# Optimization experiments

Hardware: AMD Instinct MI355X
Metric: run time of the kernel (lower is better)

Reference implementation:

```python
import jax, jax.numpy as jnp
import numpy as np

B, C, H = 4, 64, 48
HEADS, BSWIN = 2, 4
BIG = [3, 6, 12, 24]      # big window edge per scale (cubic)
SMALL = [1, 2, 4, 8]      # small (pool) window edge per scale
NH = 3                    # small windows per big window per dim (= big/small)
L = NH ** 3               # tokens per big window after pooling
CPH = C // (HEADS * BSWIN)  # channels per head per scale = 8


def _rel_pos_index():
    coords = np.stack(np.meshgrid(*([np.arange(NH)] * 3), indexing='ij')).reshape(3, -1)
    rel = coords[:, :, None] - coords[:, None, :] + (NH - 1)
    span = 2 * NH - 1
    return jnp.asarray(rel[0] * span * span + rel[1] * span + rel[2])  # (L, L) int

REL_IDX = _rel_pos_index()


def _interp_matrix(n_in, n_out):
    # 1D linear interpolation matrix, align_corners=True (matches F.interpolate)
    if n_out == n_in:
        return jnp.eye(n_in, dtype=jnp.float32)
    pos = jnp.arange(n_out, dtype=jnp.float32) * (n_in - 1) / (n_out - 1)
    i0 = jnp.clip(jnp.floor(pos).astype(jnp.int32), 0, n_in - 2)
    w = pos - i0.astype(jnp.float32)
    r = jnp.arange(n_out)
    m = jnp.zeros((n_out, n_in), jnp.float32)
    return m.at[r, i0].add(1.0 - w).at[r, i0 + 1].add(w)


def _gather(x):
    # x: (B, C, H, H, H) -> (B, HEADS, sum_N, L, CPH)
    b = x.shape[0]
    x = x.reshape(b, BSWIN, HEADS, CPH, H, H, H)
    parts, Ns = [], []
    for i in range(BSWIN):
        bw, sw = BIG[i], SMALL[i]
        N1 = H // bw
        xi = x[:, i].reshape(b, HEADS, CPH, N1, NH, sw, N1, NH, sw, N1, NH, sw)
        xi = xi.max(axis=(5, 8, 11))  # max-pool each small window
        # (b, head, c, Nh, nh, Nw, nw, Nd, nd) -> b head (Nh Nw Nd) (nh nw nd) c
        xi = xi.transpose(0, 1, 3, 5, 7, 4, 6, 8, 2)
        parts.append(xi.reshape(b, HEADS, N1 ** 3, L, CPH))
        Ns.append(N1)
    return jnp.concatenate(parts, axis=2), Ns


def _scatter(attn, Ns):
    # attn: (B, HEADS, sum_N, L, CPH) -> (B, C, H, H, H)
    b = attn.shape[0]
    outs, idx = [], 0
    for i in range(BSWIN):
        bw, sw = BIG[i], SMALL[i]
        N1 = Ns[i]
        N = N1 ** 3
        o = attn[:, :, idx:idx + N].reshape(b, HEADS, N, NH, NH, NH, CPH)
        M = _interp_matrix(NH, bw)  # trilinear upsample by small window size
        o = jnp.einsum('bhnijkc,pi,qj,rk->bhnpqrc', o, M, M, M)
        o = o.reshape(b, HEADS, N1, N1, N1, bw, bw, bw, CPH)
        # b head Nh Nw Nd wh ww wd c -> b head c (Nh wh) (Nw ww) (Nd wd)
        o = o.transpose(0, 1, 8, 2, 5, 3, 6, 4, 7).reshape(b, HEADS, CPH, H, H, H)
        outs.append(o)
        idx += N
    out = jnp.stack(outs, axis=1)  # b bswin head c h w d
    return out.reshape(b, C, H, H, H)


def _attention(q, k, v, rpb_table):
    c = q.shape[-1]
    scores = jnp.einsum('bhNmc,bhNnc->bhNmn', q, k) / jnp.sqrt(jnp.asarray(c, q.dtype))
    w = jax.nn.softmax(scores, axis=-1)
    bias = rpb_table[REL_IDX].transpose(2, 0, 1)  # (head, L, L), added POST-softmax
    w = w + bias[None, :, None]
    return jnp.einsum('bhNmn,bhNnc->bhNmc', w, v)


def setup_inputs() -> dict:
    key = jax.random.key(0)
    kq, kk, kv, kp = jax.random.split(key, 4)
    shp = (B, C, H, H, H)
    return {
        'query': jax.random.normal(kq, shp, jnp.float32),
        'key': jax.random.normal(kk, shp, jnp.float32),
        'value': jax.random.normal(kv, shp, jnp.float32),
        'rpb_table': jax.random.normal(kp, ((2 * NH - 1) ** 3, HEADS), jnp.float32) * 0.02,
    }


def reference(query, key, value, rpb_table):
    q, Ns = _gather(query)
    k, _ = _gather(key)
    v, _ = _gather(value)
    attn = _attention(q, k, v, rpb_table)
    return _scatter(attn, Ns)
```

## Files before the change

kernel.cpp:

```cpp
#include <hip/hip_runtime.h>


static constexpr long S1 = 4L * 48 * 24 * 24 * 24;
static constexpr long S2 = 4L * 32 * 12 * 12 * 12;
static constexpr long S3 = 4L * 16 * 6 * 6 * 6;

template <int OUTW>
__global__ void pool_kernel(const float* __restrict__ in0,
                            const float* __restrict__ in1,
                            const float* __restrict__ in2,
                            float* __restrict__ out, long outStride,
                            int Cin, int chOff, int Cout, int Din, int n)
{
    const float* in = blockIdx.y == 0 ? in0 : (blockIdx.y == 1 ? in1 : in2);
    float* o = out + (long)blockIdx.y * outStride;
    const int Dout = Din >> 1;
    const int QX = Dout / OUTW;
    int idx = blockIdx.x * blockDim.x + threadIdx.x;
    if (idx >= n) return;
    int qx = idx % QX;
    int t = idx / QX;
    int y = t % Dout; t /= Dout;
    int z = t % Dout; t /= Dout;
    int c = t % Cout;
    int b = t / Cout;
    const float* p = in + ((((long)b * Cin + c + chOff) * Din + 2 * z) * Din + 2 * y) * Din
                        + qx * (2 * OUTW);
    const float* rows[4] = { p, p + Din, p + (long)Din * Din, p + (long)Din * Din + Din };

    float v[4][2 * OUTW];
#pragma unroll
    for (int r = 0; r < 4; r++) {
#pragma unroll
        for (int j = 0; j < OUTW / 2; j++) {
            float4 f = *(const float4*)(rows[r] + 4 * j);
            v[r][4 * j + 0] = f.x; v[r][4 * j + 1] = f.y;
            v[r][4 * j + 2] = f.z; v[r][4 * j + 3] = f.w;
        }
    }
    float res[OUTW];
#pragma unroll
    for (int i = 0; i < OUTW; i++) {
        float m0 = fmaxf(v[0][2 * i], v[0][2 * i + 1]);
        float m1 = fmaxf(v[1][2 * i], v[1][2 * i + 1]);
        float m2 = fmaxf(v[2][2 * i], v[2][2 * i + 1]);
        float m3 = fmaxf(v[3][2 * i], v[3][2 * i + 1]);
        res[i] = fmaxf(fmaxf(m0, m1), fmaxf(m2, m3));
    }
    long oaddr = ((((long)b * Cout + c) * Dout + z) * Dout + y) * Dout + qx * OUTW;
    if (OUTW == 4) {
        *(float4*)(o + oaddr) = make_float4(res[0], res[1], res[2], res[3 % OUTW]);
    } else {
        *(float2*)(o + oaddr) = make_float2(res[0], res[1]);
    }
}

template <int S>
__global__ void attn_kernel(const float* __restrict__ qsrc,
                            const float* __restrict__ ksrc,
                            const float* __restrict__ vsrc,
                            const float* __restrict__ rpb,
                            float* __restrict__ attnOut)
{
    constexpr int N1 = (S == 0 ? 16 : S == 1 ? 8 : S == 2 ? 4 : 2);
    constexpr int D  = 3 * N1;
    constexpr int Cs = (S == 0 ? 64 : S == 1 ? 48 : S == 2 ? 32 : 16);
    constexpr int scaleOff = (S == 0 ? 0 : S == 1 ? 4096 : S == 2 ? 4608 : 4672);
    constexpr int VEC = (S == 3 ? 2 : 4);
    constexpr int SEG = 3 * D;
    constexpr int NSEG = 72;
    constexpr int TOTV = NSEG * SEG / VEC;

    __shared__ float tile[N1][3][27][8];
    __shared__ float bias_lds[2][27][27];

    const int b = blockIdx.z;
    const int head = blockIdx.y;
    const int Wz = blockIdx.x / N1;
    const int Wy = blockIdx.x % N1;

    for (int i = threadIdx.x; i < 2 * 729; i += blockDim.x) {
        int h = i / 729;
        int mn = i % 729;
        int m = mn / 27, n = mn % 27;
        int mi = m / 9, mj = (m / 3) % 3, mk = m % 3;
        int ni = n / 9, nj = (n / 3) % 3, nk = n % 3;
        int ridx = (mi - ni + 2) * 25 + (mj - nj + 2) * 5 + (mk - nk + 2);
        bias_lds[h][m][n] = rpb[ridx * 2 + h];
    }

    for (int i = threadIdx.x; i < TOTV; i += blockDim.x) {
        int seg = i / (SEG / VEC);
        int off = (i % (SEG / VEC)) * VEC;
        int tz = seg / 24;
        int rem = seg % 24;
        int cph = rem / 3;
        int zt = rem % 3;
        const float* src = tz == 0 ? qsrc : (tz == 1 ? ksrc : vsrc);
        long base = ((((long)b * Cs + head * 8 + cph) * D + (3 * Wz + zt)) * D + 3 * Wy) * (long)D;
        const float* sp = src + base + off;
        float vals[VEC];
        if (VEC == 4) {
            float4 f = *(const float4*)sp;
            vals[0] = f.x; vals[1] = f.y; vals[2] = f.z; vals[3 % VEC] = f.w;
        } else {
            float2 f = *(const float2*)sp;
            vals[0] = f.x; vals[1] = f.y;
        }
#pragma unroll
        for (int j = 0; j < VEC; j++) {
            int f = off + j;
            int r = f / D;
            int x = f % D;
            tile[x / 3][tz][zt * 9 + r * 3 + (x % 3)][cph] = vals[j];
        }
    }
    __syncthreads();

    const int wx = threadIdx.x >> 5;
    const int lane = threadIdx.x & 31;
    if (lane >= 27) return;
    const int m = lane;

    float qr[8];
#pragma unroll
    for (int c = 0; c < 8; c++) qr[c] = tile[wx][0][m][c];

    float s[27];
    float mx = -1e30f;
#pragma unroll
    for (int n = 0; n < 27; n++) {
        float acc = 0.f;
#pragma unroll
        for (int c = 0; c < 8; c++) acc += qr[c] * tile[wx][1][n][c];
        acc *= 0.35355339059327373f;
        s[n] = acc;
        mx = fmaxf(mx, acc);
    }
    float sum = 0.f;
#pragma unroll
    for (int n = 0; n < 27; n++) {
        s[n] = __expf(s[n] - mx);
        sum += s[n];
    }
    float rs = 1.0f / sum;

    float o[8] = {0, 0, 0, 0, 0, 0, 0, 0};
#pragma unroll
    for (int n = 0; n < 27; n++) {
        float wgt = s[n] * rs + bias_lds[head][m][n];
#pragma unroll
        for (int c = 0; c < 8; c++) o[c] += wgt * tile[wx][2][n][c];
    }

    const int win = (Wz * N1 + Wy) * N1 + wx;
    float* dst = attnOut + (((long)(b * 2 + head) * 4680 + scaleOff + win) * 27 + m) * 8;
    *(float4*)(dst) = make_float4(o[0], o[1], o[2], o[3]);
    *(float4*)(dst + 4) = make_float4(o[4], o[5], o[6], o[7]);
}

template <int S>
__global__ void scatter_s(const float* __restrict__ attn, float* __restrict__ out)
{
    constexpr int bw = (S == 0 ? 3 : S == 1 ? 6 : S == 2 ? 12 : 24);
    constexpr int N1 = 48 / bw;
    constexpr int scaleOff = (S == 0 ? 0 : S == 1 ? 4096 : S == 2 ? 4608 : 4672);
    constexpr int CZ = (S == 0 ? 3 : S == 1 ? 3 : 1);
    constexpr int NZC = bw / CZ;
    constexpr int LDSF = N1 * 216;
    constexpr int NF4 = CZ * bw * 8 * 12;

    __shared__ float lds[LDSF];

    const int b = blockIdx.z;
    const int head = blockIdx.y;
    int t = blockIdx.x;
    const int zc = t % NZC; t /= NZC;
    const int Wy = t % N1;
    const int Wz = t / N1;

    const float* src = attn + ((long)(b * 2 + head) * 4680 + scaleOff + (Wz * N1 + Wy) * N1) * 216;
    for (int i = threadIdx.x; i < LDSF / 4; i += blockDim.x)
        *(float4*)(lds + 4 * i) = *(const float4*)(src + 4 * i);
    __syncthreads();

    const float inv = 2.0f / (float)(bw - 1);

    for (int i = threadIdx.x; i < NF4; i += blockDim.x) {
        int x4 = i % 12;
        int t2 = i / 12;
        int cph = t2 % 8; t2 /= 8;
        int y = t2 % bw;
        int zl = t2 / bw;
        int wp = zc * CZ + zl;

        float4 res;
        float* rr = (float*)&res;

        if (S == 0) {
#pragma unroll
            for (int e = 0; e < 4; e++) {
                int r = x4 * 4 + e;
                int Wx = r / 3, wr = r % 3;
                rr[e] = lds[(Wx * 27 + (wp * 3 + y) * 3 + wr) * 8 + cph];
            }
        } else {
            float posp = wp * inv; int i0p = min((int)posp, 1); float fp = posp - (float)i0p;
            float posq = y * inv;  int i0q = min((int)posq, 1); float fq = posq - (float)i0q;
            float wpv[2] = {1.f - fp, fp};
            float wqv[2] = {1.f - fq, fq};
#pragma unroll
            for (int e = 0; e < 4; e++) {
                int r = x4 * 4 + e;
                int Wx = r / bw, wr = r % bw;
                float posr = wr * inv; int i0r = min((int)posr, 1); float fr = posr - (float)i0r;
                float wrv[2] = {1.f - fr, fr};
                const float* basep = lds + Wx * 216 + cph;
                float acc = 0.f;
#pragma unroll
                for (int di = 0; di < 2; di++) {
#pragma unroll
                    for (int dj = 0; dj < 2; dj++) {
#pragma unroll
                        for (int dk = 0; dk < 2; dk++) {
                            int tok = ((i0p + di) * 3 + (i0q + dj)) * 3 + (i0r + dk);
                            acc += wpv[di] * wqv[dj] * wrv[dk] * basep[tok * 8];
                        }
                    }
                }
                rr[e] = acc;
            }
        }

        int z = Wz * bw + wp;
        int Y = Wy * bw + y;
        long oaddr = (((long)(b * 64 + S * 16 + head * 8 + cph) * 48 + z) * 48 + Y) * 48 + x4 * 4;
        *(float4*)(out + oaddr) = res;
    }
}

extern "C" void kernel_launch(void* const* d_in, const int* in_sizes, int n_in,
                              void* d_out, int out_size, void* d_ws, size_t ws_size,
                              hipStream_t stream)
{
    const float* q   = (const float*)d_in[0];
    const float* k   = (const float*)d_in[1];
    const float* v   = (const float*)d_in[2];
    const float* rpb = (const float*)d_in[3];
    float* out = (float*)d_out;

    float* ws = (float*)d_ws;
    float* P1 = ws;
    float* P2 = ws + 3 * S1;
    float* P3 = ws + 3 * S1 + 3 * S2;
    float* attn = ws + 3 * S1 + 3 * S2 + 3 * S3;

    {
        const int n1 = 4 * 48 * 24 * 24 * 6;
        dim3 g1((n1 + 255) / 256, 3);
        pool_kernel<4><<<g1, 256, 0, stream>>>(q, k, v, P1, S1, 64, 16, 48, 48, n1);

        const int n2 = 4 * 32 * 12 * 12 * 3;
        dim3 g2((n2 + 255) / 256, 3);
        pool_kernel<4><<<g2, 256, 0, stream>>>(P1, P1 + S1, P1 + 2 * S1, P2, S2, 48, 16, 32, 24, n2);

        const int n3 = 4 * 16 * 6 * 6 * 3;
        dim3 g3((n3 + 255) / 256, 3);
        pool_kernel<2><<<g3, 256, 0, stream>>>(P2, P2 + S2, P2 + 2 * S2, P3, S3, 32, 16, 16, 12, n3);
    }

    attn_kernel<0><<<dim3(256, 2, 4), 512, 0, stream>>>(q, k, v, rpb, attn);
    attn_kernel<1><<<dim3(64, 2, 4), 256, 0, stream>>>(P1, P1 + S1, P1 + 2 * S1, rpb, attn);
    attn_kernel<2><<<dim3(16, 2, 4), 128, 0, stream>>>(P2, P2 + S2, P2 + 2 * S2, rpb, attn);
    attn_kernel<3><<<dim3(4, 2, 4), 64, 0, stream>>>(P3, P3 + S3, P3 + 2 * S3, rpb, attn);

    scatter_s<0><<<dim3(16 * 16 * 1, 2, 4), 256, 0, stream>>>(attn, out);
    scatter_s<1><<<dim3(8 * 8 * 2, 2, 4), 256, 0, stream>>>(attn, out);
    scatter_s<2><<<dim3(4 * 4 * 12, 2, 4), 256, 0, stream>>>(attn, out);
    scatter_s<3><<<dim3(2 * 2 * 24, 2, 4), 256, 0, stream>>>(attn, out);
}
```

Before: 200.4 us.

## Add LDS-staged first-level pool kernel and merge four scatter launches into one

Replaces the generic first 2x2x2 max-pool launch with a dedicated kernel. It loads four input z-planes with coalesced float4 reads, reduces along x on the fly into LDS, then finishes the y/z reduction from LDS. It also folds the four per-scale scatter kernels into a single launch that picks the scale from the block index, which removes three launches and lets the scales run concurrently. In exchange, every scatter block now reserves the largest LDS buffer, and the merged kernel's register use is set by the heaviest scale.

```diff
diff --git a/kernel.cpp b/kernel.cpp
--- a/kernel.cpp
+++ b/kernel.cpp
@@ -4,6 +4,60 @@
 static constexpr long S1 = 4L * 48 * 24 * 24 * 24;
 static constexpr long S2 = 4L * 32 * 12 * 12 * 12;
 static constexpr long S3 = 4L * 16 * 6 * 6 * 6;
+
+__global__ void pool48_kernel(const float* __restrict__ in0,
+                              const float* __restrict__ in1,
+                              const float* __restrict__ in2,
+                              float* __restrict__ out, long outStride)
+{
+    constexpr int ZPB = 2;
+    constexpr int PLANES = 2 * ZPB;
+    constexpr int RSTRIDE = 28;
+    __shared__ float xp[PLANES * 48 * RSTRIDE];
+
+    const float* in = blockIdx.y == 0 ? in0 : (blockIdx.y == 1 ? in1 : in2);
+    float* o = out + (long)blockIdx.y * outStride;
+
+    int bx = blockIdx.x;
+    const int zc = bx % 12; bx /= 12;
+    const int c = bx % 48;
+    const int b = bx / 48;
+    const int zIn0 = zc * PLANES;
+
+    const float* base = in + ((long)b * 64 + 16 + c) * 110592 + (long)zIn0 * 2304;
+
+    for (int i = threadIdx.x; i < PLANES * 48 * 12; i += 256) {
+        int p = i / 576;
+        int rem = i % 576;
+        int r = rem / 12;
+        int x4 = rem % 12;
+        float4 f = *(const float4*)(base + (long)p * 2304 + r * 48 + 4 * x4);
+        float2 m = make_float2(fmaxf(f.x, f.y), fmaxf(f.z, f.w));
+        *(float2*)(&xp[(p * 48 + r) * RSTRIDE + 2 * x4]) = m;
+    }
+    __syncthreads();
+
+    for (int i = threadIdx.x; i < ZPB * 144; i += 256) {
+        int zl = i / 144;
+        int rem = i % 144;
+        int oy = rem / 6;
+        int ox4 = rem % 6;
+        const float* p0 = &xp[((2 * zl) * 48 + 2 * oy) * RSTRIDE + 4 * ox4];
+        const float* p1 = p0 + RSTRIDE;
+        const float* p2 = p0 + 48 * RSTRIDE;
+        const float* p3 = p2 + RSTRIDE;
+        float4 a = *(const float4*)p0;
+        float4 bb = *(const float4*)p1;
+        float4 cc = *(const float4*)p2;
+        float4 d = *(const float4*)p3;
+        float4 r4 = make_float4(fmaxf(fmaxf(a.x, bb.x), fmaxf(cc.x, d.x)),
+                                fmaxf(fmaxf(a.y, bb.y), fmaxf(cc.y, d.y)),
+                                fmaxf(fmaxf(a.z, bb.z), fmaxf(cc.z, d.z)),
+                                fmaxf(fmaxf(a.w, bb.w), fmaxf(cc.w, d.w)));
+        long oaddr = (((long)b * 48 + c) * 24 + (zc * ZPB + zl)) * 576 + oy * 24 + 4 * ox4;
+        *(float4*)(o + oaddr) = r4;
+    }
+}
 
 template <int OUTW>
 __global__ void pool_kernel(const float* __restrict__ in0,
@@ -160,7 +214,10 @@
 }
 
 template <int S>
-__global__ void scatter_s(const float* __restrict__ attn, float* __restrict__ out)
+__device__ __forceinline__ void scatter_impl(const float* __restrict__ attn,
+                                             float* __restrict__ out,
+                                             float* lds, int t, int b, int head,
+                                             int tid)
 {
     constexpr int bw = (S == 0 ? 3 : S == 1 ? 6 : S == 2 ? 12 : 24);
     constexpr int N1 = 48 / bw;
@@ -170,23 +227,18 @@
     constexpr int LDSF = N1 * 216;
     constexpr int NF4 = CZ * bw * 8 * 12;
 
-    __shared__ float lds[LDSF];
-
-    const int b = blockIdx.z;
-    const int head = blockIdx.y;
-    int t = blockIdx.x;
     const int zc = t % NZC; t /= NZC;
     const int Wy = t % N1;
     const int Wz = t / N1;
 
     const float* src = attn + ((long)(b * 2 + head) * 4680 + scaleOff + (Wz * N1 + Wy) * N1) * 216;
-    for (int i = threadIdx.x; i < LDSF / 4; i += blockDim.x)
+    for (int i = tid; i < LDSF / 4; i += 256)
         *(float4*)(lds + 4 * i) = *(const float4*)(src + 4 * i);
     __syncthreads();
 
     const float inv = 2.0f / (float)(bw - 1);
 
-    for (int i = threadIdx.x; i < NF4; i += blockDim.x) {
+    for (int i = tid; i < NF4; i += 256) {
         int x4 = i % 12;
         int t2 = i / 12;
         int cph = t2 % 8; t2 /= 8;
@@ -239,6 +291,19 @@
     }
 }
 
+__global__ void scatter_all(const float* __restrict__ attn, float* __restrict__ out)
+{
+    __shared__ float lds[16 * 216];
+    const int b = blockIdx.z;
+    const int head = blockIdx.y;
+    const int bx = blockIdx.x;
+    const int tid = threadIdx.x;
+    if (bx < 256)      scatter_impl<0>(attn, out, lds, bx,       b, head, tid);
+    else if (bx < 384) scatter_impl<1>(attn, out, lds, bx - 256, b, head, tid);
+    else if (bx < 576) scatter_impl<2>(attn, out, lds, bx - 384, b, head, tid);
+    else               scatter_impl<3>(attn, out, lds, bx - 576, b, head, tid);
+}
+
 extern "C" void kernel_launch(void* const* d_in, const int* in_sizes, int n_in,
                               void* d_out, int out_size, void* d_ws, size_t ws_size,
                               hipStream_t stream)
@@ -255,11 +320,9 @@
     float* P3 = ws + 3 * S1 + 3 * S2;
     float* attn = ws + 3 * S1 + 3 * S2 + 3 * S3;
 
+    pool48_kernel<<<dim3(4 * 48 * 12, 3), 256, 0, stream>>>(q, k, v, P1, S1);
+
     {
-        const int n1 = 4 * 48 * 24 * 24 * 6;
-        dim3 g1((n1 + 255) / 256, 3);
-        pool_kernel<4><<<g1, 256, 0, stream>>>(q, k, v, P1, S1, 64, 16, 48, 48, n1);
-
         const int n2 = 4 * 32 * 12 * 12 * 3;
         dim3 g2((n2 + 255) / 256, 3);
         pool_kernel<4><<<g2, 256, 0, stream>>>(P1, P1 + S1, P1 + 2 * S1, P2, S2, 48, 16, 32, 24, n2);
@@ -274,8 +337,5 @@
     attn_kernel<2><<<dim3(16, 2, 4), 128, 0, stream>>>(P2, P2 + S2, P2 + 2 * S2, rpb, attn);
     attn_kernel<3><<<dim3(4, 2, 4), 64, 0, stream>>>(P3, P3 + S3, P3 + 2 * S3, rpb, attn);
 
-    scatter_s<0><<<dim3(16 * 16 * 1, 2, 4), 256, 0, stream>>>(attn, out);
-    scatter_s<1><<<dim3(8 * 8 * 2, 2, 4), 256, 0, stream>>>(attn, out);
-    scatter_s<2><<<dim3(4 * 4 * 12, 2, 4), 256, 0, stream>>>(attn, out);
-    scatter_s<3><<<dim3(2 * 2 * 24, 2, 4), 256, 0, stream>>>(attn, out);
-}
+    scatter_all<<<dim3(672, 2, 4), 256, 0, stream>>>(attn, out);
+}
```

New measurement: 188.7 us. -5.8%, faster.
